# Performance work log

Hardware: AMD Instinct MI355X
Metric: run time of the kernel (lower is better)

The kernel has to match this reference:

```python
import jax, jax.numpy as jnp
import numpy as np

GRID_SIZE = 5
G1 = GRID_SIZE + 1
GRID = jnp.linspace(-1.0, 1.0, G1)
INV2SIG2 = 0.5 * GRID_SIZE ** 2  # 1/(2*sigma^2), sigma = 1/grid_size
L = 3      # num_layers
NH = 8     # num_heads
C = 256    # feature_dim
HID = 1024 # hidden_dim


def kan(x, bw, sw):
    # x: (T, in), bw: (out, in), sw: (out, in, G1)
    base = x @ bw.T
    bases = jnp.exp(-((x[..., None] - GRID) ** 2) * INV2SIG2)  # (T, in, G1)
    bases = bases / (bases.sum(-1, keepdims=True) + 1e-8)
    return base + jnp.einsum('big,oig->bo', bases, sw)


def layernorm(x, g, b, eps=1e-5):
    m = x.mean(-1, keepdims=True)
    v = x.var(-1, keepdims=True)
    return (x - m) / jnp.sqrt(v + eps) * g + b


def gelu(x):
    return jax.nn.gelu(x, approximate=False)


def _forward(sat_features, uav_features,
             sat_qkvp_base, sat_qkvp_spline, sat_rp_base, sat_rp_spline,
             uav_qkvp_base, uav_qkvp_spline, uav_rp_base, uav_rp_spline,
             ref_w1_base, ref_w1_spline, ref_w2_base, ref_w2_spline, ref_ln_g, ref_ln_b,
             sim_w1_base, sim_w1_spline, sim_w2_base, sim_w2_spline, sim_w3_base, sim_w3_spline,
             fus_w_base, fus_w_spline, fus_ln_g, fus_ln_b):
    B, Cc, H, W = sat_features.shape
    N = H * W
    HD = Cc // NH
    scale = HD ** -0.5
    sat = sat_features.reshape(B, Cc, N).transpose(0, 2, 1)  # (B, N, C)
    uav = uav_features.reshape(B, Cc, N).transpose(0, 2, 1)

    # relative coords (same geometry every layer)
    ch = jnp.arange(H)
    cw = jnp.arange(W)
    coords = jnp.stack(jnp.meshgrid(ch, cw, indexing='ij')).reshape(2, N)  # (2, N)
    rel = (coords[:, :, None] - coords[:, None, :]).transpose(1, 2, 0).astype(jnp.float32)  # (N, N, 2)
    rel = rel / jnp.array([H - 1.0, W - 1.0], dtype=jnp.float32)
    rel_flat = rel.reshape(-1, 2)

    def attn_block(x, qb, qs, rb, rs):
        xf = x.reshape(-1, Cc)
        q = kan(xf, qb[0], qs[0]).reshape(B, N, NH, HD).transpose(0, 2, 1, 3)
        k = kan(xf, qb[1], qs[1]).reshape(B, N, NH, HD).transpose(0, 2, 1, 3)
        v = kan(xf, qb[2], qs[2]).reshape(B, N, NH, HD).transpose(0, 2, 1, 3)
        bias = kan(rel_flat, rb, rs).reshape(N, N, NH).transpose(2, 0, 1)  # (NH, N, N)
        a = jnp.einsum('bhnd,bhmd->bhnm', q, k) * scale + bias[None]
        a = jax.nn.softmax(a, axis=-1)
        o = jnp.einsum('bhnm,bhmd->bhnd', a, v).transpose(0, 2, 1, 3).reshape(B, N, Cc)
        return kan(o.reshape(-1, Cc), qb[3], qs[3]).reshape(B, N, Cc)

    def refine(x, i):
        xf = x.reshape(-1, Cc)
        h = gelu(kan(xf, ref_w1_base[i], ref_w1_spline[i]))
        h = kan(h, ref_w2_base[i], ref_w2_spline[i])
        h = layernorm(h, ref_ln_g[i], ref_ln_b[i])
        return h.reshape(x.shape)

    for i in range(L):
        se = attn_block(sat, sat_qkvp_base[i], sat_qkvp_spline[i], sat_rp_base[i], sat_rp_spline[i])
        ue = attn_block(uav, uav_qkvp_base[i], uav_qkvp_spline[i], uav_rp_base[i], uav_rp_spline[i])
        sat = se + refine(se, i)
        uav = ue + refine(ue, i)

    sg = sat.mean(1)  # (B, C)
    ug = uav.mean(1)
    si = jnp.concatenate([sg, ug], axis=1)
    h = gelu(kan(si, sim_w1_base, sim_w1_spline))
    h = gelu(kan(h, sim_w2_base, sim_w2_spline))
    w = jax.nn.sigmoid(kan(h, sim_w3_base, sim_w3_spline))  # (B, 1)
    fi = jnp.concatenate([sg * w, ug * (1.0 - w)], axis=1)
    out = gelu(layernorm(kan(fi, fus_w_base, fus_w_spline), fus_ln_g, fus_ln_b))
    return out


def setup_inputs() -> dict:
    key = jax.random.key(0)
    ks = jax.random.split(key, 32)
    B, H, W = 8, 24, 24
    n = lambda k, shape, s=0.05: jax.random.normal(k, shape, dtype=jnp.float32) * s
    inp = {
        'sat_features': jax.random.normal(ks[0], (B, C, H, W), dtype=jnp.float32),
        'uav_features': jax.random.normal(ks[1], (B, C, H, W), dtype=jnp.float32),
        'sat_qkvp_base': n(ks[2], (L, 4, C, C)),
        'sat_qkvp_spline': n(ks[3], (L, 4, C, C, G1), 0.01),
        'sat_rp_base': n(ks[4], (L, NH, 2)),
        'sat_rp_spline': n(ks[5], (L, NH, 2, G1), 0.01),
        'uav_qkvp_base': n(ks[6], (L, 4, C, C)),
        'uav_qkvp_spline': n(ks[7], (L, 4, C, C, G1), 0.01),
        'uav_rp_base': n(ks[8], (L, NH, 2)),
        'uav_rp_spline': n(ks[9], (L, NH, 2, G1), 0.01),
        'ref_w1_base': n(ks[10], (L, HID, C)),
        'ref_w1_spline': n(ks[11], (L, HID, C, G1), 0.01),
        'ref_w2_base': n(ks[12], (L, C, HID)),
        'ref_w2_spline': n(ks[13], (L, C, HID, G1), 0.01),
        'ref_ln_g': jnp.ones((L, C), jnp.float32),
        'ref_ln_b': jnp.zeros((L, C), jnp.float32),
        'sim_w1_base': n(ks[14], (HID, 2 * C)),
        'sim_w1_spline': n(ks[15], (HID, 2 * C, G1), 0.01),
        'sim_w2_base': n(ks[16], (C // 4, HID)),
        'sim_w2_spline': n(ks[17], (C // 4, HID, G1), 0.01),
        'sim_w3_base': n(ks[18], (1, C // 4)),
        'sim_w3_spline': n(ks[19], (1, C // 4, G1), 0.01),
        'fus_w_base': n(ks[20], (C, 2 * C)),
        'fus_w_spline': n(ks[21], (C, 2 * C, G1), 0.01),
        'fus_ln_g': jnp.ones((C,), jnp.float32),
        'fus_ln_b': jnp.zeros((C,), jnp.float32),
    }
    return inp


def reference(sat_features, uav_features,
              sat_qkvp_base, sat_qkvp_spline, sat_rp_base, sat_rp_spline,
              uav_qkvp_base, uav_qkvp_spline, uav_rp_base, uav_rp_spline,
              ref_w1_base, ref_w1_spline, ref_w2_base, ref_w2_spline, ref_ln_g, ref_ln_b,
              sim_w1_base, sim_w1_spline, sim_w2_base, sim_w2_spline, sim_w3_base, sim_w3_spline,
              fus_w_base, fus_w_spline, fus_ln_g, fus_ln_b):
    return _forward(sat_features, uav_features,
                    sat_qkvp_base, sat_qkvp_spline, sat_rp_base, sat_rp_spline,
                    uav_qkvp_base, uav_qkvp_spline, uav_rp_base, uav_rp_spline,
                    ref_w1_base, ref_w1_spline, ref_w2_base, ref_w2_spline, ref_ln_g, ref_ln_b,
                    sim_w1_base, sim_w1_spline, sim_w2_base, sim_w2_spline, sim_w3_base, sim_w3_spline,
                    fus_w_base, fus_w_spline, fus_ln_g, fus_ln_b)
```

## Files before the change

### kernel.cpp

```cpp
#include <hip/hip_runtime.h>
#include <math.h>

#define TT      4608
#define BB      8
#define NTOK    576
#define CDIM    256
#define NHEADS  8
#define HIDDIM  1024

typedef __attribute__((ext_vector_type(8))) short bf8s;
typedef __attribute__((ext_vector_type(4))) float f4;
typedef __attribute__((ext_vector_type(4))) short sv4;
typedef __attribute__((ext_vector_type(8))) short sv8;

__device__ __forceinline__ f4 mfma16(bf8s a, bf8s b, f4 c) {
    return __builtin_amdgcn_mfma_f32_16x16x32_bf16(a, b, c, 0, 0, 0);
}

__device__ __forceinline__ unsigned short f2bf(float x) {
    union { float f; unsigned int u; } v; v.f = x;
    unsigned int r = v.u + 0x7FFFu + ((v.u >> 16) & 1u);
    return (unsigned short)(r >> 16);
}
__device__ __forceinline__ float bf2f(unsigned short h) {
    union { unsigned int u; float f; } v; v.u = ((unsigned int)h) << 16;
    return v.f;
}
__device__ __forceinline__ unsigned int cvtpk(float a, float b) {
    unsigned int r;
    asm("v_cvt_pk_bf16_f32 %0, %1, %2" : "=v"(r) : "v"(a), "v"(b));
    return r;
}

__device__ __forceinline__ float gelu_f(float x) {
    return 0.5f * x * (1.0f + erff(x * 0.70710678118654752f));
}

__device__ __forceinline__ void bases6(float v, float* out) {
    float vc = fminf(fmaxf(v, -1.6f), 1.6f);
    float t = fmaf(vc, 10.f, 10.f);
    float r = __expf(t);
    float e0 = 1.f;
    float e1 = r * 1.3533528e-1f;
    float e2 = e1 * (r * 2.4787522e-3f);
    float e3 = e2 * (r * 4.5399930e-5f);
    float e4 = e3 * (r * 8.3152872e-7f);
    float e5 = e4 * (r * 1.5229979e-8f);
    float av = fmaxf(fabsf(v) - 1.f, 0.f);
    float g = __expf(fminf(fmaf(av * av, 12.5f, -18.420681f), 80.f));
    float inv = 1.f / ((e0 + e1 + e2 + e3 + e4 + e5) * (1.f + g));
    out[0] = e0 * inv; out[1] = e1 * inv; out[2] = e2 * inv;
    out[3] = e3 * inv; out[4] = e4 * inv; out[5] = e5 * inv;
}

__device__ __forceinline__ int4 expand_pack(float v) {
    float b6[6]; bases6(v, b6);
    int4 pk;
    pk.x = (int)cvtpk(v, b6[0]);
    pk.y = (int)cvtpk(b6[1], b6[2]);
    pk.z = (int)cvtpk(b6[3], b6[4]);
    pk.w = (int)cvtpk(b6[5], 0.f);
    return pk;
}

__device__ __forceinline__ void gload16(const void* g, void* l) {
    __builtin_amdgcn_global_load_lds(
        (const __attribute__((address_space(1))) unsigned int*)g,
        (__attribute__((address_space(3))) unsigned int*)l, 16, 0, 0);
}

__global__ __launch_bounds__(256) void k_transpose(const float* __restrict__ in,
                                                   float* __restrict__ out) {
    int idx = blockIdx.x * 256 + threadIdx.x;
    if (idx >= TT * CDIM) return;
    int t = idx >> 8, c = idx & 255;
    int b = t / NTOK, n = t % NTOK;
    out[idx] = in[(b * CDIM + c) * NTOK + n];
}

__global__ __launch_bounds__(256) void k_reduceS(const unsigned short* __restrict__ p,
                                                 float4* __restrict__ out, int n4, int S) {
    int i = blockIdx.x * 256 + threadIdx.x;
    if (i >= n4) return;
    float a0 = 0.f, a1 = 0.f, a2 = 0.f, a3 = 0.f;
    for (int s = 0; s < S; s++) {
        sv4 v = *(const sv4*)(p + (size_t)s * n4 * 4 + (size_t)i * 4);
        a0 += bf2f((unsigned short)v[0]); a1 += bf2f((unsigned short)v[1]);
        a2 += bf2f((unsigned short)v[2]); a3 += bf2f((unsigned short)v[3]);
    }
    out[i] = make_float4(a0, a1, a2, a3);
}

__global__ __launch_bounds__(256) void k_reduce_exp(const unsigned short* __restrict__ p,
                                                    float4* __restrict__ seb,
                                                    unsigned short* __restrict__ aexp,
                                                    int n4, int S) {
    int i = blockIdx.x * 256 + threadIdx.x;
    if (i >= n4) return;
    float a0 = 0.f, a1 = 0.f, a2 = 0.f, a3 = 0.f;
    for (int s = 0; s < S; s++) {
        sv4 v = *(const sv4*)(p + (size_t)s * n4 * 4 + (size_t)i * 4);
        a0 += bf2f((unsigned short)v[0]); a1 += bf2f((unsigned short)v[1]);
        a2 += bf2f((unsigned short)v[2]); a3 += bf2f((unsigned short)v[3]);
    }
    seb[i] = make_float4(a0, a1, a2, a3);
    int t = i >> 6, i4 = (i & 63) << 2;
    float xa[4] = {a0, a1, a2, a3};
#pragma unroll
    for (int u = 0; u < 4; u++) {
        int4 pk = expand_pack(xa[u]);
        *(int4*)(aexp + (size_t)t * 2048 + (size_t)(i4 + u) * 8) = pk;
    }
}

__global__ __launch_bounds__(256) void k_expand8(const float* __restrict__ x,
                                                 unsigned short* __restrict__ out, int Mr) {
    int idx = blockIdx.x * 256 + threadIdx.x;
    if (idx >= Mr * 64) return;
    int t = idx >> 6, i4 = (idx & 63) << 2;
    float4 xv = *(const float4*)(x + (size_t)t * 256 + i4);
    float xa[4] = {xv.x, xv.y, xv.z, xv.w};
#pragma unroll
    for (int u = 0; u < 4; u++) {
        int4 pk = expand_pack(xa[u]);
        *(int4*)(out + (size_t)t * 2048 + (size_t)(i4 + u) * 8) = pk;
    }
}

__global__ __launch_bounds__(256) void k_pack8(
    const float* __restrict__ sqb, const float* __restrict__ sqs,
    const float* __restrict__ uqb, const float* __restrict__ uqs,
    const float* __restrict__ w1b, const float* __restrict__ w1s,
    const float* __restrict__ w2b, const float* __restrict__ w2s,
    unsigned short* __restrict__ Wq, unsigned short* __restrict__ Wp,
    unsigned short* __restrict__ Ww1, unsigned short* __restrict__ Ww2) {
    const size_t gQ = 196608, gP = 65536, g1 = 262144;
    const int ly = blockIdx.y;
    const size_t bofs = (size_t)ly * 262144, sofs = (size_t)ly * 1572864;
    size_t idx = (size_t)blockIdx.x * 256 + threadIdx.x;
    const float* base; const float* spl; unsigned short* dst; size_t off;
    if (idx < 2 * gQ) {
        int s = idx >= gQ; off = idx - (size_t)s * gQ;
        base = (s ? uqb : sqb) + bofs; spl = (s ? uqs : sqs) + sofs;
        dst = Wq + (size_t)ly * 3145728 + (size_t)s * gQ * 8;
    } else if (idx < 2 * gQ + 2 * gP) {
        size_t o2 = idx - 2 * gQ; int s = o2 >= gP; off = o2 - (size_t)s * gP;
        base = (s ? uqb : sqb) + bofs + 3 * 65536;
        spl  = (s ? uqs : sqs) + sofs + 3 * 393216;
        dst = Wp + (size_t)ly * 1048576 + (size_t)s * gP * 8;
    } else if (idx < 2 * gQ + 2 * gP + g1) {
        off = idx - 2 * gQ - 2 * gP;
        base = w1b + bofs; spl = w1s + sofs; dst = Ww1 + (size_t)ly * 2097152;
    } else {
        off = idx - 2 * gQ - 2 * gP - g1;
        base = w2b + bofs; spl = w2s + sofs; dst = Ww2 + (size_t)ly * 2097152;
    }
    float bv = base[off];
    float2 s01 = *(const float2*)(spl + off * 6);
    float2 s23 = *(const float2*)(spl + off * 6 + 2);
    float2 s45 = *(const float2*)(spl + off * 6 + 4);
    int4 pk;
    pk.x = (int)cvtpk(bv, s01.x);
    pk.y = (int)cvtpk(s01.y, s23.x);
    pk.z = (int)cvtpk(s23.y, s45.x);
    pk.w = (int)cvtpk(s45.y, 0.f);
    *(int4*)(dst + off * 8) = pk;
}

template<int BM, int BN, int ACT, int CMODE, int EXP>
__global__ __launch_bounds__(256) void mgemm(const void* __restrict__ Araw,
                                             const unsigned short* __restrict__ W0,
                                             const unsigned short* __restrict__ W1,
                                             void* __restrict__ Cv, int NN, int K,
                                             int ALD, int WLD, int gx, int groupRows,
                                             int S, int Kc, size_t skStride) {
    constexpr int MF = BM / 32;
    constexpr int NF = BN / 32;
    constexpr int PD = 4;
    __shared__ unsigned short As[2][BM * 32];
    __shared__ unsigned short Bs[2][BN * 32];
    int nwg = gridDim.x, orig = blockIdx.x;
    int q = nwg >> 3, r = nwg & 7;
    int xcd = orig & 7, loc = orig >> 3;
    int wg = (xcd < r ? xcd * (q + 1) : r * (q + 1) + (xcd - r) * q) + loc;
    int sk = wg % S; int rest = wg / S;
    int bx = rest % gx, by = rest / gx;
    const int bm = by * BM, bn = bx * BN;
    const unsigned short* W = (bm >= groupRows) ? W1 : W0;
    const int tid = threadIdx.x, l = tid & 63, w = tid >> 6;
    const int wr = w >> 1, wc = w & 1;
    const int sr = l >> 2;
    const int scg = (l & 3) ^ ((l >> 3) & 3);
    const int sc8 = scg * 8;
    const int fro = (l & 15) * 32 + (((l >> 4) ^ ((l >> 1) & 3)) << 3);
    const int k0 = sk * Kc;
    f4 acc[MF][NF];
#pragma unroll
    for (int m = 0; m < MF; m++)
#pragma unroll
        for (int n = 0; n < NF; n++) acc[m][n] = (f4){0.f, 0.f, 0.f, 0.f};

    const unsigned short* Abf = (const unsigned short*)Araw;
    float xvr[PD][BM / 64];
    auto loadXd = [&](int kt, int slot) {
#pragma unroll
        for (int it = 0; it < BM / 64; it++) {
            int ch = it * 4 + w;
            int row = bm + ch * 16 + sr;
            int xi = (kt >> 3) + scg;
            xvr[slot][it] = bf2f(Abf[(size_t)row * ALD + xi]);
        }
    };
    auto writeA = [&](int buf, int slot) {
#pragma unroll
        for (int it = 0; it < BM / 64; it++) {
            int ch = it * 4 + w;
            int4 pk = expand_pack(xvr[slot][it]);
            *(int4*)&As[buf][ch * 512 + l * 8] = pk;
        }
    };
    auto stageA = [&](int buf, int kt) {
#pragma unroll
        for (int it = 0; it < BM / 64; it++) {
            int ch = it * 4 + w;
            gload16(Abf + (size_t)(bm + ch * 16 + sr) * ALD + kt + sc8,
                    (void*)(&As[buf][ch * 512 + l * 8]));
        }
    };
    auto stageB = [&](int buf, int kt) {
#pragma unroll
        for (int it = 0; it < BN / 64; it++) {
            int ch = it * 4 + w;
            gload16(W + (size_t)(bn + ch * 16 + sr) * WLD + kt + sc8,
                    (void*)(&Bs[buf][ch * 512 + l * 8]));
        }
    };

    const int nt = Kc / 32;
    if constexpr (EXP == 0) {
        stageA(0, k0);
    } else {
        int npre = nt < PD ? nt : PD;
        for (int d = 0; d < npre; d++) loadXd(k0 + d * 32, d);
        writeA(0, 0);
    }
    stageB(0, k0);
    __syncthreads();
    for (int t = 0; t < nt; t++) {
        int cur = t & 1;
        if (t + 1 < nt) {
            if constexpr (EXP == 0) stageA(cur ^ 1, k0 + (t + 1) * 32);
            stageB(cur ^ 1, k0 + (t + 1) * 32);
        }
        if constexpr (EXP != 0) {
            if (t + PD < nt) loadXd(k0 + (t + PD) * 32, (t + PD) & (PD - 1));
        }
        bf8s af[MF], bfr[NF];
#pragma unroll
        for (int m = 0; m < MF; m++)
            af[m] = *(const bf8s*)&As[cur][(wr * MF + m) * 512 + fro];
#pragma unroll
        for (int n = 0; n < NF; n++)
            bfr[n] = *(const bf8s*)&Bs[cur][(wc * NF + n) * 512 + fro];
#pragma unroll
        for (int m = 0; m < MF; m++)
#pragma unroll
            for (int n = 0; n < NF; n++)
                acc[m][n] = mfma16(af[m], bfr[n], acc[m][n]);
        if constexpr (EXP != 0) { if (t + 1 < nt) writeA(cur ^ 1, (t + 1) & (PD - 1)); }
        __syncthreads();
    }
#pragma unroll
    for (int m = 0; m < MF; m++)
#pragma unroll
        for (int n = 0; n < NF; n++)
#pragma unroll
            for (int j = 0; j < 4; j++) {
                int row = bm + wr * (BM / 2) + m * 16 + (l >> 4) * 4 + j;
                int col = bn + wc * (BN / 2) + n * 16 + (l & 15);
                float v = acc[m][n][j];
                if (ACT == 1) v = gelu_f(v);
                size_t o = (size_t)row * NN + col;
                if (CMODE == 0)      ((float*)Cv)[(size_t)sk * skStride + o] = v;
                else if (CMODE == 5) ((unsigned short*)Cv)[(size_t)sk * skStride + o] = f2bf(v);
                else                 ((unsigned short*)Cv)[o] = f2bf(v);
            }
}

__global__ __launch_bounds__(256) void k_vt(const unsigned short* __restrict__ QKV,
                                            unsigned short* __restrict__ VT) {
    const int n0 = blockIdx.x * 64, h = blockIdx.y, z = blockIdx.z;
    __shared__ unsigned short t[32][72];
    const int tid = threadIdx.x;
    {
        int nl = tid >> 2, d8 = (tid & 3) * 8;
        sv8 v = *(const sv8*)(QKV + ((size_t)z * 576 + n0 + nl) * 768 + 512 + h * 32 + d8);
#pragma unroll
        for (int j = 0; j < 8; j++) t[d8 + j][nl] = v[j];
    }
    __syncthreads();
    {
        int d = tid >> 3, n8 = (tid & 7) * 8;
        sv8 o;
#pragma unroll
        for (int j = 0; j < 8; j++) o[j] = t[d][n8 + j];
        *(sv8*)(VT + ((size_t)(z * 8 + h) * 32 + d) * 576 + n0 + n8) = o;
    }
}

__global__ __launch_bounds__(256) void k_bias_tab(const float* __restrict__ rb0,
                                                  const float* __restrict__ rs0,
                                                  const float* __restrict__ rb1,
                                                  const float* __restrict__ rs1,
                                                  float* __restrict__ Btab) {
    int sidx = blockIdx.y;
    const float* rb = sidx ? rb1 : rb0;
    const float* rs = sidx ? rs1 : rs0;
    float* B = Btab + (size_t)sidx * NHEADS * 2209;
    int idx = blockIdx.x * 256 + threadIdx.x;
    if (idx >= 2209) return;
    float r0 = (float)(idx / 47 - 23) * (1.0f / 23.0f);
    float r1 = (float)(idx % 47 - 23) * (1.0f / 23.0f);
    float v[2][6];
    bases6(r0, v[0]);
    bases6(r1, v[1]);
#pragma unroll
    for (int h = 0; h < NHEADS; h++) {
        float s = rb[h * 2] * r0 + rb[h * 2 + 1] * r1;
#pragma unroll
        for (int g = 0; g < 6; g++)
            s += rs[h * 12 + g] * v[0][g] + rs[h * 12 + 6 + g] * v[1][g];
        B[(size_t)h * 2209 + idx] = s;
    }
}

__global__ __launch_bounds__(256) void k_attn2(const unsigned short* __restrict__ QKV,
                                               const unsigned short* __restrict__ VT,
                                               const float* __restrict__ Btab,
                                               unsigned short* __restrict__ AX) {
    int nwg = gridDim.x, orig = blockIdx.x;
    int qq = nwg >> 3, rr_ = nwg & 7;
    int xcd = orig & 7, loc = orig >> 3;
    int wg = (xcd < rr_ ? xcd * (qq + 1) : rr_ * (qq + 1) + (xcd - rr_) * qq) + loc;
    const int n0 = (wg % 18) * 32;
    const int h = (wg / 18) & 7;
    const int z = wg / 144;
    const int tid = threadIdx.x, l = tid & 63, w = tid >> 6;
    const int rh = (w & 1) * 16;
    const int kh = (w >> 1) * 16;
    __shared__ unsigned short Ps[4][32 * 40];
    __shared__ float red[4][16];
    __shared__ float bt[2209];
    const float scale = 0.17677669529663687f;
    const size_t rowbase = (size_t)z * NTOK;
    const float* Bh = Btab + ((size_t)(z >> 3) * NHEADS + h) * 2209;
    for (int i = tid; i < 2209; i += 256) bt[i] = Bh[i];
    const unsigned short* VTh = VT + ((size_t)(z * 8 + h) * 32) * 576;

    bf8s qf = *(const bf8s*)(QKV + (rowbase + n0 + rh + (l & 15)) * 768 + h * 32 + (l >> 4) * 8);

    f4 s[18];
#pragma unroll
    for (int kc = 0; kc < 18; kc++) {
        bf8s kf = *(const bf8s*)(QKV + (rowbase + kc * 32 + kh + (l & 15)) * 768 + 256 + h * 32 + (l >> 4) * 8);
        f4 zz = {0.f, 0.f, 0.f, 0.f};
        s[kc] = mfma16(qf, kf, zz);
    }
    __syncthreads();

    const int r0 = n0 + rh + (l >> 4) * 4;
    int bidx[4];
#pragma unroll
    for (int j = 0; j < 4; j++) {
        int n = r0 + j;
        bidx[j] = (n / 24 + 23) * 47 + (n % 24 + 23);
    }
    int m0 = kh + (l & 15);
    int mq = (m0 >= 24) ? 1 : 0;
    int mr = m0 - 24 * mq;
    float mx[4] = {-1e30f, -1e30f, -1e30f, -1e30f};
#pragma unroll
    for (int kc = 0; kc < 18; kc++) {
        int moff = mq * 47 + mr;
        mr += 8; mq += 1;
        if (mr >= 24) { mr -= 24; mq += 1; }
#pragma unroll
        for (int j = 0; j < 4; j++) {
            float v = s[kc][j] * scale + bt[bidx[j] - moff];
            s[kc][j] = v;
            mx[j] = fmaxf(mx[j], v);
        }
    }
#pragma unroll
    for (int j = 0; j < 4; j++)
#pragma unroll
        for (int m = 1; m < 16; m <<= 1) mx[j] = fmaxf(mx[j], __shfl_xor(mx[j], m));
    if ((l & 15) == 0) {
#pragma unroll
        for (int j = 0; j < 4; j++) red[w][(l >> 4) * 4 + j] = mx[j];
    }
    __syncthreads();
#pragma unroll
    for (int j = 0; j < 4; j++) mx[j] = fmaxf(mx[j], red[w ^ 2][(l >> 4) * 4 + j]);
    __syncthreads();
    float sm[4] = {0.f, 0.f, 0.f, 0.f};
#pragma unroll
    for (int kc = 0; kc < 18; kc++)
#pragma unroll
        for (int j = 0; j < 4; j++) {
            float p = __expf(s[kc][j] - mx[j]);
            s[kc][j] = p;
            sm[j] += p;
        }
#pragma unroll
    for (int j = 0; j < 4; j++)
#pragma unroll
        for (int m = 1; m < 16; m <<= 1) sm[j] += __shfl_xor(sm[j], m);
    if ((l & 15) == 0) {
#pragma unroll
        for (int j = 0; j < 4; j++) red[w][(l >> 4) * 4 + j] = sm[j];
    }
    __syncthreads();
#pragma unroll
    for (int j = 0; j < 4; j++) sm[j] = 1.f / (sm[j] + red[w ^ 2][(l >> 4) * 4 + j]);

    f4 oacc = {0.f, 0.f, 0.f, 0.f};
#pragma unroll
    for (int kc2 = 0; kc2 < 18; kc2 += 2) {
        const int b0 = kc2 & 2;
#pragma unroll
        for (int u = 0; u < 2; u++) {
            int kc = kc2 + u;
#pragma unroll
            for (int j = 0; j < 4; j++)
                Ps[b0 + u][(rh + (l >> 4) * 4 + j) * 40 + kh + (l & 15)] = f2bf(s[kc][j]);
        }
        __syncthreads();
#pragma unroll
        for (int u = 0; u < 2; u++) {
            int kc = kc2 + u;
            bf8s pf = *(const bf8s*)&Ps[b0 + u][(rh + (l & 15)) * 40 + (l >> 4) * 8];
            bf8s vf = *(const bf8s*)(VTh + (size_t)(kh + (l & 15)) * 576 + kc * 32 + (l >> 4) * 8);
            oacc = mfma16(pf, vf, oacc);
        }
    }
#pragma unroll
    for (int j = 0; j < 4; j++) {
        float ov = oacc[j] * sm[j];
        int4 pk = expand_pack(ov);
        *(int4*)(AX + ((rowbase + n0 + rh + (l >> 4) * 4 + j) * 2048
                       + (size_t)(h * 32 + kh + (l & 15)) * 8)) = pk;
    }
}

__global__ __launch_bounds__(256) void k_ln_addS(const unsigned short* __restrict__ P,
                                                 int S, size_t st,
                                                 const float* __restrict__ SE,
                                                 const float* __restrict__ g,
                                                 const float* __restrict__ bb,
                                                 float* __restrict__ Out,
                                                 unsigned short* __restrict__ aexp,
                                                 int doExp) {
    int t = blockIdx.x, c = threadIdx.x;
    size_t o = (size_t)t * 256 + c;
    float v = 0.f;
    for (int s = 0; s < S; s++) v += bf2f(P[o + (size_t)s * st]);
    float s1 = v, s2 = v * v;
#pragma unroll
    for (int off = 32; off; off >>= 1) { s1 += __shfl_xor(s1, off); s2 += __shfl_xor(s2, off); }
    __shared__ float p1[4], p2[4];
    int wv_ = c >> 6, ln = c & 63;
    if (ln == 0) { p1[wv_] = s1; p2[wv_] = s2; }
    __syncthreads();
    s1 = p1[0] + p1[1] + p1[2] + p1[3];
    s2 = p2[0] + p2[1] + p2[2] + p2[3];
    float m = s1 * (1.f / 256.f);
    float var = s2 * (1.f / 256.f) - m * m;
    float y = (v - m) * rsqrtf(var + 1e-5f) * g[c] + bb[c];
    float xn = SE[o] + y;
    Out[o] = xn;
    if (doExp) {
        int4 pk = expand_pack(xn);
        *(int4*)(aexp + (size_t)t * 2048 + (size_t)c * 8) = pk;
    }
}

__global__ __launch_bounds__(256) void k_ln_gelu(const float* __restrict__ Xin,
                                                 const float* __restrict__ g,
                                                 const float* __restrict__ bb,
                                                 float* __restrict__ Out) {
    int t = blockIdx.x, c = threadIdx.x;
    float v = Xin[t * 256 + c];
    float s1 = v, s2 = v * v;
#pragma unroll
    for (int off = 32; off; off >>= 1) { s1 += __shfl_xor(s1, off); s2 += __shfl_xor(s2, off); }
    __shared__ float p1[4], p2[4];
    int wv_ = c >> 6, ln = c & 63;
    if (ln == 0) { p1[wv_] = s1; p2[wv_] = s2; }
    __syncthreads();
    s1 = p1[0] + p1[1] + p1[2] + p1[3];
    s2 = p2[0] + p2[1] + p2[2] + p2[3];
    float m = s1 * (1.f / 256.f);
    float var = s2 * (1.f / 256.f) - m * m;
    float y = (v - m) * rsqrtf(var + 1e-5f) * g[c] + bb[c];
    Out[t * 256 + c] = gelu_f(y);
}

__global__ __launch_bounds__(256) void k_meanpool(const float* __restrict__ X,
                                                  float* __restrict__ si, int colofs) {
    int idx = blockIdx.x * 256 + threadIdx.x;
    if (idx >= BB * CDIM) return;
    int b = idx >> 8, c = idx & 255;
    float s = 0.f;
    for (int n = 0; n < NTOK; n++) s += X[(size_t)(b * NTOK + n) * CDIM + c];
    si[b * 512 + colofs + c] = s * (1.f / 576.f);
}

__global__ __launch_bounds__(256) void k_expand(const float* __restrict__ x,
                                                float* __restrict__ bases, int total) {
    int idx = blockIdx.x * 256 + threadIdx.x;
    if (idx >= total) return;
    float b6[6];
    bases6(x[idx], b6);
#pragma unroll
    for (int g = 0; g < 6; g++) bases[idx * 6 + g] = b6[g];
}

__global__ __launch_bounds__(64) void k_small_kan(const float* __restrict__ A1, int K1,
                                                  const float* __restrict__ A2, int K2,
                                                  const float* __restrict__ W1,
                                                  const float* __restrict__ W2,
                                                  float* __restrict__ out, int NN, int act) {
    int o = blockIdx.x, t = blockIdx.y, ln = threadIdx.x;
    float s = 0.f;
    for (int k = ln; k < K1; k += 64) s += A1[t * K1 + k] * W1[o * K1 + k];
    for (int k = ln; k < K2; k += 64) s += A2[t * K2 + k] * W2[o * K2 + k];
#pragma unroll
    for (int off = 32; off; off >>= 1) s += __shfl_xor(s, off);
    if (ln == 0) {
        if (act == 1) s = gelu_f(s);
        else if (act == 2) s = 1.f / (1.f + __expf(-s));
        out[t * NN + o] = s;
    }
}

__global__ void k_fi(const float* __restrict__ si, const float* __restrict__ wv,
                     float* __restrict__ fi) {
    int idx = blockIdx.x * 256 + threadIdx.x;
    if (idx >= BB * 512) return;
    int b = idx >> 9, i = idx & 511;
    float w = wv[b];
    fi[idx] = si[idx] * (i < 256 ? w : 1.f - w);
}

extern "C" void kernel_launch(void* const* d_in, const int* in_sizes, int n_in,
                              void* d_out, int out_size, void* d_ws, size_t ws_size,
                              hipStream_t stream) {
    (void)in_sizes; (void)n_in; (void)out_size;
    const float* sat_f = (const float*)d_in[0];
    const float* uav_f = (const float*)d_in[1];
    const float* s_qb  = (const float*)d_in[2];
    const float* s_qs  = (const float*)d_in[3];
    const float* s_rb  = (const float*)d_in[4];
    const float* s_rs  = (const float*)d_in[5];
    const float* u_qb  = (const float*)d_in[6];
    const float* u_qs  = (const float*)d_in[7];
    const float* u_rb  = (const float*)d_in[8];
    const float* u_rs  = (const float*)d_in[9];
    const float* r_w1b = (const float*)d_in[10];
    const float* r_w1s = (const float*)d_in[11];
    const float* r_w2b = (const float*)d_in[12];
    const float* r_w2s = (const float*)d_in[13];
    const float* r_lng = (const float*)d_in[14];
    const float* r_lnb = (const float*)d_in[15];
    const float* m_w1b = (const float*)d_in[16];
    const float* m_w1s = (const float*)d_in[17];
    const float* m_w2b = (const float*)d_in[18];
    const float* m_w2s = (const float*)d_in[19];
    const float* m_w3b = (const float*)d_in[20];
    const float* m_w3s = (const float*)d_in[21];
    const float* f_wb  = (const float*)d_in[22];
    const float* f_ws  = (const float*)d_in[23];
    const float* f_lng = (const float*)d_in[24];
    const float* f_lnb = (const float*)d_in[25];

    const size_t nQ = 1572864, nP = 524288;

    float* X; unsigned short* QKVb; unsigned short* VT; char* R; float* PS;
    unsigned short* AEXP;
    unsigned short *Wq, *Wp, *Ww1, *Ww2;
    float *Btab, *si, *SB, *h1f, *h2f, *wvv, *fiB, *ftmp;
    auto plan = [&](int nb, bool ded, bool pall, bool assign) -> size_t {
        size_t off = 0;
        auto take = [&](size_t bytes) -> char* {
            char* rp = (char*)d_ws + off;
            off = (off + bytes + 255) & ~(size_t)255;
            return rp;
        };
        size_t Mr = (size_t)nb * TT;
        int nl = pall ? 3 : 1;
        char* p;
        p = take((size_t)2 * TT * 256 * 4);             if (assign) X = (float*)p;
        p = take(Mr * 768 * 2);                         if (assign) QKVb = (unsigned short*)p;
        p = take(Mr * 256 * 2);                         if (assign) VT = (unsigned short*)p;
        p = take(Mr * 2048 * 2);                        if (assign) R = p;
        p = take((size_t)4 * Mr * 256 * 4);             if (assign) PS = (float*)p;
        if (ded) { p = take(Mr * 2048 * 2);             if (assign) AEXP = (unsigned short*)p; }
        else     { if (assign) AEXP = (unsigned short*)PS; }
        p = take((size_t)nl * 2 * nQ * 2);              if (assign) Wq = (unsigned short*)p;
        p = take((size_t)nl * 2 * nP * 2);              if (assign) Wp = (unsigned short*)p;
        p = take((size_t)nl * 2097152 * 2);             if (assign) Ww1 = (unsigned short*)p;
        p = take((size_t)nl * 2097152 * 2);             if (assign) Ww2 = (unsigned short*)p;
        p = take((size_t)nb * NHEADS * 2209 * 4);       if (assign) Btab = (float*)p;
        p = take(BB * 512 * 4);                         if (assign) si = (float*)p;
        p = take((size_t)BB * 1024 * 6 * 4);            if (assign) SB = (float*)p;
        p = take(BB * 1024 * 4);                        if (assign) h1f = (float*)p;
        p = take(BB * 64 * 4);                          if (assign) h2f = (float*)p;
        p = take(64 * 4);                               if (assign) wvv = (float*)p;
        p = take(BB * 512 * 4);                         if (assign) fiB = (float*)p;
        p = take(BB * 256 * 4);                         if (assign) ftmp = (float*)p;
        return off;
    };
    int nb; bool ded, pall;
    if      (ws_size >= plan(2, true,  true,  false)) { nb = 2; ded = true;  pall = true;  }
    else if (ws_size >= plan(2, true,  false, false)) { nb = 2; ded = true;  pall = false; }
    else if (ws_size >= plan(2, false, false, false)) { nb = 2; ded = false; pall = false; }
    else                                              { nb = 1; ded = true;  pall = false; }
    plan(nb, ded, pall, true);
    const bool fuseRed = ded;
    const bool fuseLn  = ded && (nb == 2);

    k_transpose<<<TT, 256, 0, stream>>>(sat_f, X);
    k_transpose<<<TT, 256, 0, stream>>>(uav_f, X + (size_t)TT * 256);

    const int Mr = nb * TT;
    const size_t pStride = (size_t)Mr * 256;
    unsigned short* AEXPp = (unsigned short*)R;
    unsigned short* H1bp  = (unsigned short*)R;
    float* SEbp = (float*)(R + (size_t)Mr * 1024 * 2);

    if (pall)
        k_pack8<<<dim3(4096, 3), 256, 0, stream>>>(s_qb, s_qs, u_qb, u_qs,
                                                   r_w1b, r_w1s, r_w2b, r_w2s,
                                                   Wq, Wp, Ww1, Ww2);

    for (int l = 0; l < 3; l++) {
        if (!pall)
            k_pack8<<<dim3(4096, 1), 256, 0, stream>>>(
                s_qb + (size_t)l * 262144, s_qs + (size_t)l * 1572864,
                u_qb + (size_t)l * 262144, u_qs + (size_t)l * 1572864,
                r_w1b + (size_t)l * 262144, r_w1s + (size_t)l * 1572864,
                r_w2b + (size_t)l * 262144, r_w2s + (size_t)l * 1572864,
                Wq, Wp, Ww1, Ww2);
        unsigned short* WqL  = Wq  + (pall ? (size_t)l * 2 * nQ : 0);
        unsigned short* WpL  = Wp  + (pall ? (size_t)l * 2 * nP : 0);
        unsigned short* Ww1L = Ww1 + (pall ? (size_t)l * 2097152 : 0);
        unsigned short* Ww2L = Ww2 + (pall ? (size_t)l * 2097152 : 0);

        for (int st0 = 0; st0 < 2; st0 += nb) {
            float* Xs = X + (size_t)st0 * TT * 256;
            bool haveAexp = fuseLn && (l > 0);
            if (!haveAexp) k_expand8<<<Mr / 4, 256, 0, stream>>>(Xs, AEXP, Mr);
            mgemm<128, 128, 0, 2, 0><<<6 * (Mr / 128), 256, 0, stream>>>(
                AEXP, WqL + (size_t)st0 * nQ, WqL + nQ, (void*)QKVb,
                768, 2048, 2048, 2048, 6, TT, 1, 2048, 0);
            k_vt<<<dim3(9, 8, nb * 8), 256, 0, stream>>>(QKVb, VT);
            {
                const float* rbA = (st0 ? u_rb : s_rb) + l * 16;
                const float* rsA = (st0 ? u_rs : s_rs) + l * 96;
                k_bias_tab<<<dim3(9, nb), 256, 0, stream>>>(rbA, rsA, u_rb + l * 16, u_rs + l * 96, Btab);
            }
            k_attn2<<<144 * nb * 8, 256, 0, stream>>>(QKVb, VT, Btab, AEXPp);
            mgemm<128, 128, 0, 5, 0><<<2 * (Mr / 128) * 4, 256, 0, stream>>>(
                AEXPp, WpL + (size_t)st0 * nP, WpL + nP, (void*)PS,
                256, 2048, 2048, 2048, 2, TT, 4, 512, pStride);
            if (fuseRed)
                k_reduce_exp<<<Mr / 4, 256, 0, stream>>>((const unsigned short*)PS, (float4*)SEbp, AEXP, Mr * 64, 4);
            else {
                k_reduceS<<<Mr / 4, 256, 0, stream>>>((const unsigned short*)PS, (float4*)SEbp, Mr * 64, 4);
                k_expand8<<<Mr / 4, 256, 0, stream>>>(SEbp, AEXP, Mr);
            }
            mgemm<128, 128, 1, 2, 0><<<8 * (Mr / 128), 256, 0, stream>>>(
                AEXP, Ww1L, Ww1L, (void*)H1bp,
                1024, 2048, 2048, 2048, 8, TT, 1, 2048, 0);
            mgemm<64, 256, 0, 5, 2><<<4 * (Mr / 64), 256, 0, stream>>>(
                H1bp, Ww2L, Ww2L, (void*)PS,
                256, 8192, 1024, 8192, 1, TT, 4, 2048, pStride);
            k_ln_addS<<<Mr, 256, 0, stream>>>((const unsigned short*)PS, 4, pStride, SEbp,
                                              r_lng + l * 256, r_lnb + l * 256, Xs,
                                              AEXP, (fuseLn && l < 2) ? 1 : 0);
        }
    }

    k_meanpool<<<8, 256, 0, stream>>>(X, si, 0);
    k_meanpool<<<8, 256, 0, stream>>>(X + (size_t)TT * 256, si, 256);
    k_expand<<<(BB * 512 + 255) / 256, 256, 0, stream>>>(si, SB, BB * 512);
    k_small_kan<<<dim3(1024, BB), 64, 0, stream>>>(si, 512, SB, 3072, m_w1b, m_w1s, h1f, 1024, 1);
    k_expand<<<(BB * 1024 + 255) / 256, 256, 0, stream>>>(h1f, SB, BB * 1024);
    k_small_kan<<<dim3(64, BB), 64, 0, stream>>>(h1f, 1024, SB, 6144, m_w2b, m_w2s, h2f, 64, 1);
    k_expand<<<(BB * 64 + 255) / 256, 256, 0, stream>>>(h2f, SB, BB * 64);
    k_small_kan<<<dim3(1, BB), 64, 0, stream>>>(h2f, 64, SB, 384, m_w3b, m_w3s, wvv, 1, 2);
    k_fi<<<16, 256, 0, stream>>>(si, wvv, fiB);
    k_expand<<<(BB * 512 + 255) / 256, 256, 0, stream>>>(fiB, SB, BB * 512);
    k_small_kan<<<dim3(256, BB), 64, 0, stream>>>(fiB, 512, SB, 3072, f_wb, f_ws, ftmp, 256, 0);
    k_ln_gelu<<<8, 256, 0, stream>>>(ftmp, f_lng, f_lnb, (float*)d_out);
}
```

Measured before the change: 1.073 ms.

## Pack KAN activations and weights densely as 7 columns instead of padded 8

New measurement: 1.014 ms, median of 3. 5.5% less time.

```diff
diff --git a/kernel.cpp b/kernel.cpp
--- a/kernel.cpp
+++ b/kernel.cpp
@@ -63,6 +63,15 @@
     return pk;
 }
 
+__device__ __forceinline__ void expand_cat1(float v, unsigned short* rowp, int col) {
+    rowp[col] = f2bf(v);
+    float b6[6]; bases6(v, b6);
+    int* ip = (int*)(rowp + 256 + (size_t)col * 6);
+    ip[0] = (int)cvtpk(b6[0], b6[1]);
+    ip[1] = (int)cvtpk(b6[2], b6[3]);
+    ip[2] = (int)cvtpk(b6[4], b6[5]);
+}
+
 __device__ __forceinline__ void gload16(const void* g, void* l) {
     __builtin_amdgcn_global_load_lds(
         (const __attribute__((address_space(1))) unsigned int*)g,
@@ -106,11 +115,20 @@
     seb[i] = make_float4(a0, a1, a2, a3);
     int t = i >> 6, i4 = (i & 63) << 2;
     float xa[4] = {a0, a1, a2, a3};
+    unsigned short* rowp = aexp + (size_t)t * 1792;
+    sv4 xs;
+    unsigned short tmp[24];
 #pragma unroll
     for (int u = 0; u < 4; u++) {
-        int4 pk = expand_pack(xa[u]);
-        *(int4*)(aexp + (size_t)t * 2048 + (size_t)(i4 + u) * 8) = pk;
-    }
+        xs[u] = (short)f2bf(xa[u]);
+        float b6[6]; bases6(xa[u], b6);
+#pragma unroll
+        for (int g = 0; g < 6; g++) tmp[u * 6 + g] = f2bf(b6[g]);
+    }
+    *(sv4*)(rowp + i4) = xs;
+    sv8* bp = (sv8*)(rowp + 256 + (size_t)i4 * 6);
+#pragma unroll
+    for (int k = 0; k < 3; k++) bp[k] = *(sv8*)&tmp[k * 8];
 }
 
 __global__ __launch_bounds__(256) void k_expand8(const float* __restrict__ x,
@@ -120,11 +138,20 @@
     int t = idx >> 6, i4 = (idx & 63) << 2;
     float4 xv = *(const float4*)(x + (size_t)t * 256 + i4);
     float xa[4] = {xv.x, xv.y, xv.z, xv.w};
+    unsigned short* rowp = out + (size_t)t * 1792;
+    sv4 xs;
+    unsigned short tmp[24];
 #pragma unroll
     for (int u = 0; u < 4; u++) {
-        int4 pk = expand_pack(xa[u]);
-        *(int4*)(out + (size_t)t * 2048 + (size_t)(i4 + u) * 8) = pk;
-    }
+        xs[u] = (short)f2bf(xa[u]);
+        float b6[6]; bases6(xa[u], b6);
+#pragma unroll
+        for (int g = 0; g < 6; g++) tmp[u * 6 + g] = f2bf(b6[g]);
+    }
+    *(sv4*)(rowp + i4) = xs;
+    sv8* bp = (sv8*)(rowp + 256 + (size_t)i4 * 6);
+#pragma unroll
+    for (int k = 0; k < 3; k++) bp[k] = *(sv8*)&tmp[k * 8];
 }
 
 __global__ __launch_bounds__(256) void k_pack8(
@@ -134,37 +161,61 @@
     const float* __restrict__ w2b, const float* __restrict__ w2s,
     unsigned short* __restrict__ Wq, unsigned short* __restrict__ Wp,
     unsigned short* __restrict__ Ww1, unsigned short* __restrict__ Ww2) {
-    const size_t gQ = 196608, gP = 65536, g1 = 262144;
+    const size_t B1 = 688128, B2 = 917504, B3 = 1376256;
     const int ly = blockIdx.y;
     const size_t bofs = (size_t)ly * 262144, sofs = (size_t)ly * 1572864;
     size_t idx = (size_t)blockIdx.x * 256 + threadIdx.x;
-    const float* base; const float* spl; unsigned short* dst; size_t off;
-    if (idx < 2 * gQ) {
-        int s = idx >= gQ; off = idx - (size_t)s * gQ;
-        base = (s ? uqb : sqb) + bofs; spl = (s ? uqs : sqs) + sofs;
-        dst = Wq + (size_t)ly * 3145728 + (size_t)s * gQ * 8;
-    } else if (idx < 2 * gQ + 2 * gP) {
-        size_t o2 = idx - 2 * gQ; int s = o2 >= gP; off = o2 - (size_t)s * gP;
-        base = (s ? uqb : sqb) + bofs + 3 * 65536;
-        spl  = (s ? uqs : sqs) + sofs + 3 * 393216;
-        dst = Wp + (size_t)ly * 1048576 + (size_t)s * gP * 8;
-    } else if (idx < 2 * gQ + 2 * gP + g1) {
-        off = idx - 2 * gQ - 2 * gP;
-        base = w1b + bofs; spl = w1s + sofs; dst = Ww1 + (size_t)ly * 2097152;
+    if (idx < B3) {
+        const float* base; const float* spl; unsigned short* dst; size_t e;
+        if (idx < B1) {
+            e = idx * 4;
+            int s = e >= 1376256; size_t off = e - (size_t)s * 1376256;
+            int r = (int)(off / 1792), c = (int)(off % 1792);
+            base = (s ? uqb : sqb) + bofs + (size_t)r * 256;
+            spl  = (s ? uqs : sqs) + sofs + (size_t)r * 1536;
+            dst = Wq + (size_t)ly * 2752512 + e;
+            float4 v = (c < 256) ? *(const float4*)(base + c)
+                                 : *(const float4*)(spl + (c - 256));
+            int2 pk; pk.x = (int)cvtpk(v.x, v.y); pk.y = (int)cvtpk(v.z, v.w);
+            *(int2*)dst = pk;
+        } else if (idx < B2) {
+            e = (idx - B1) * 4;
+            int s = e >= 458752; size_t off = e - (size_t)s * 458752;
+            int r = (int)(off / 1792), c = (int)(off % 1792);
+            base = (s ? uqb : sqb) + bofs + 3 * 65536 + (size_t)r * 256;
+            spl  = (s ? uqs : sqs) + sofs + 3 * 393216 + (size_t)r * 1536;
+            dst = Wp + (size_t)ly * 917504 + e;
+            float4 v = (c < 256) ? *(const float4*)(base + c)
+                                 : *(const float4*)(spl + (c - 256));
+            int2 pk; pk.x = (int)cvtpk(v.x, v.y); pk.y = (int)cvtpk(v.z, v.w);
+            *(int2*)dst = pk;
+        } else {
+            e = (idx - B2) * 4;
+            int r = (int)(e / 1792), c = (int)(e % 1792);
+            base = w1b + bofs + (size_t)r * 256;
+            spl  = w1s + sofs + (size_t)r * 1536;
+            dst = Ww1 + (size_t)ly * 1835008 + e;
+            float4 v = (c < 256) ? *(const float4*)(base + c)
+                                 : *(const float4*)(spl + (c - 256));
+            int2 pk; pk.x = (int)cvtpk(v.x, v.y); pk.y = (int)cvtpk(v.z, v.w);
+            *(int2*)dst = pk;
+        }
     } else {
-        off = idx - 2 * gQ - 2 * gP - g1;
-        base = w2b + bofs; spl = w2s + sofs; dst = Ww2 + (size_t)ly * 2097152;
-    }
-    float bv = base[off];
-    float2 s01 = *(const float2*)(spl + off * 6);
-    float2 s23 = *(const float2*)(spl + off * 6 + 2);
-    float2 s45 = *(const float2*)(spl + off * 6 + 4);
-    int4 pk;
-    pk.x = (int)cvtpk(bv, s01.x);
-    pk.y = (int)cvtpk(s01.y, s23.x);
-    pk.z = (int)cvtpk(s23.y, s45.x);
-    pk.w = (int)cvtpk(s45.y, 0.f);
-    *(int4*)(dst + off * 8) = pk;
+        size_t g = idx - B3;
+        const float* base = w2b + bofs;
+        const float* spl  = w2s + sofs;
+        unsigned short* dst = Ww2 + (size_t)ly * 2097152 + g * 8;
+        float bv = base[g];
+        float2 s01 = *(const float2*)(spl + g * 6);
+        float2 s23 = *(const float2*)(spl + g * 6 + 2);
+        float2 s45 = *(const float2*)(spl + g * 6 + 4);
+        int4 pk;
+        pk.x = (int)cvtpk(bv, s01.x);
+        pk.y = (int)cvtpk(s01.y, s23.x);
+        pk.z = (int)cvtpk(s23.y, s45.x);
+        pk.w = (int)cvtpk(s45.y, 0.f);
+        *(int4*)dst = pk;
+    }
 }
 
 template<int BM, int BN, int ACT, int CMODE, int EXP>
@@ -447,9 +498,8 @@
 #pragma unroll
     for (int j = 0; j < 4; j++) {
         float ov = oacc[j] * sm[j];
-        int4 pk = expand_pack(ov);
-        *(int4*)(AX + ((rowbase + n0 + rh + (l >> 4) * 4 + j) * 2048
-                       + (size_t)(h * 32 + kh + (l & 15)) * 8)) = pk;
+        size_t rowi = rowbase + n0 + rh + (l >> 4) * 4 + j;
+        expand_cat1(ov, AX + rowi * 1792, h * 32 + kh + (l & 15));
     }
 }
 
@@ -479,10 +529,7 @@
     float y = (v - m) * rsqrtf(var + 1e-5f) * g[c] + bb[c];
     float xn = SE[o] + y;
     Out[o] = xn;
-    if (doExp) {
-        int4 pk = expand_pack(xn);
-        *(int4*)(aexp + (size_t)t * 2048 + (size_t)c * 8) = pk;
-    }
+    if (doExp) expand_cat1(xn, aexp + (size_t)t * 1792, c);
 }
 
 __global__ __launch_bounds__(256) void k_ln_gelu(const float* __restrict__ Xin,
@@ -584,7 +631,7 @@
     const float* f_lng = (const float*)d_in[24];
     const float* f_lnb = (const float*)d_in[25];
 
-    const size_t nQ = 1572864, nP = 524288;
+    const size_t nQ = 1376256, nP = 458752;
 
     float* X; unsigned short* QKVb; unsigned short* VT; char* R; float* PS;
     unsigned short* AEXP;
@@ -605,11 +652,11 @@
         p = take(Mr * 256 * 2);                         if (assign) VT = (unsigned short*)p;
         p = take(Mr * 2048 * 2);                        if (assign) R = p;
         p = take((size_t)4 * Mr * 256 * 4);             if (assign) PS = (float*)p;
-        if (ded) { p = take(Mr * 2048 * 2);             if (assign) AEXP = (unsigned short*)p; }
+        if (ded) { p = take(Mr * 1792 * 2);             if (assign) AEXP = (unsigned short*)p; }
         else     { if (assign) AEXP = (unsigned short*)PS; }
         p = take((size_t)nl * 2 * nQ * 2);              if (assign) Wq = (unsigned short*)p;
         p = take((size_t)nl * 2 * nP * 2);              if (assign) Wp = (unsigned short*)p;
-        p = take((size_t)nl * 2097152 * 2);             if (assign) Ww1 = (unsigned short*)p;
+        p = take((size_t)nl * 1835008 * 2);             if (assign) Ww1 = (unsigned short*)p;
         p = take((size_t)nl * 2097152 * 2);             if (assign) Ww2 = (unsigned short*)p;
         p = take((size_t)nb * NHEADS * 2209 * 4);       if (assign) Btab = (float*)p;
         p = take(BB * 512 * 4);                         if (assign) si = (float*)p;
@@ -640,13 +687,13 @@
     float* SEbp = (float*)(R + (size_t)Mr * 1024 * 2);
 
     if (pall)
-        k_pack8<<<dim3(4096, 3), 256, 0, stream>>>(s_qb, s_qs, u_qb, u_qs,
+        k_pack8<<<dim3(6400, 3), 256, 0, stream>>>(s_qb, s_qs, u_qb, u_qs,
                                                    r_w1b, r_w1s, r_w2b, r_w2s,
                                                    Wq, Wp, Ww1, Ww2);
 
     for (int l = 0; l < 3; l++) {
         if (!pall)
-            k_pack8<<<dim3(4096, 1), 256, 0, stream>>>(
+            k_pack8<<<dim3(6400, 1), 256, 0, stream>>>(
                 s_qb + (size_t)l * 262144, s_qs + (size_t)l * 1572864,
                 u_qb + (size_t)l * 262144, u_qs + (size_t)l * 1572864,
                 r_w1b + (size_t)l * 262144, r_w1s + (size_t)l * 1572864,
@@ -654,7 +701,7 @@
                 Wq, Wp, Ww1, Ww2);
         unsigned short* WqL  = Wq  + (pall ? (size_t)l * 2 * nQ : 0);
         unsigned short* WpL  = Wp  + (pall ? (size_t)l * 2 * nP : 0);
-        unsigned short* Ww1L = Ww1 + (pall ? (size_t)l * 2097152 : 0);
+        unsigned short* Ww1L = Ww1 + (pall ? (size_t)l * 1835008 : 0);
         unsigned short* Ww2L = Ww2 + (pall ? (size_t)l * 2097152 : 0);
 
         for (int st0 = 0; st0 < 2; st0 += nb) {
@@ -663,7 +710,7 @@
             if (!haveAexp) k_expand8<<<Mr / 4, 256, 0, stream>>>(Xs, AEXP, Mr);
             mgemm<128, 128, 0, 2, 0><<<6 * (Mr / 128), 256, 0, stream>>>(
                 AEXP, WqL + (size_t)st0 * nQ, WqL + nQ, (void*)QKVb,
-                768, 2048, 2048, 2048, 6, TT, 1, 2048, 0);
+                768, 1792, 1792, 1792, 6, TT, 1, 1792, 0);
             k_vt<<<dim3(9, 8, nb * 8), 256, 0, stream>>>(QKVb, VT);
             {
                 const float* rbA = (st0 ? u_rb : s_rb) + l * 16;
@@ -673,7 +720,7 @@
             k_attn2<<<144 * nb * 8, 256, 0, stream>>>(QKVb, VT, Btab, AEXPp);
             mgemm<128, 128, 0, 5, 0><<<2 * (Mr / 128) * 4, 256, 0, stream>>>(
                 AEXPp, WpL + (size_t)st0 * nP, WpL + nP, (void*)PS,
-                256, 2048, 2048, 2048, 2, TT, 4, 512, pStride);
+                256, 1792, 1792, 1792, 2, TT, 4, 448, pStride);
             if (fuseRed)
                 k_reduce_exp<<<Mr / 4, 256, 0, stream>>>((const unsigned short*)PS, (float4*)SEbp, AEXP, Mr * 64, 4);
             else {
@@ -682,7 +729,7 @@
             }
             mgemm<128, 128, 1, 2, 0><<<8 * (Mr / 128), 256, 0, stream>>>(
                 AEXP, Ww1L, Ww1L, (void*)H1bp,
-                1024, 2048, 2048, 2048, 8, TT, 1, 2048, 0);
+                1024, 1792, 1792, 1792, 8, TT, 1, 1792, 0);
             mgemm<64, 256, 0, 5, 2><<<4 * (Mr / 64), 256, 0, stream>>>(
                 H1bp, Ww2L, Ww2L, (void*)PS,
                 256, 8192, 1024, 8192, 1, TT, 4, 2048, pStride);
```
